# Kernel optimization log

Measured on AMD Instinct MI355X. Metric: run time of the kernel, lower is better.

The kernel has to match this reference:

```python
import jax, jax.numpy as jnp
import numpy as np

NEG_BIG = -9e15  # matches torch's -9000000000000000.0 mask value
LRELU_ALPHA = 0.2


def setup_inputs() -> dict:
    key = jax.random.key(0)
    ks = jax.random.split(key, 6)
    B, N, Fin, Fout = 2, 4096, 64, 64
    x = jax.random.normal(ks[0], (B, N, Fin), jnp.float32)
    pos = jax.random.normal(ks[1], (B, N, 3), jnp.float32)
    # xavier-ish scaled params
    W = jax.random.normal(ks[2], (Fin, Fout), jnp.float32) * (1.0 / np.sqrt(Fin))
    a = jax.random.normal(ks[3], (2 * Fout, 1), jnp.float32) * (1.0 / np.sqrt(2 * Fout))
    Wp = jax.random.normal(ks[4], (3, Fout), jnp.float32) * (1.0 / np.sqrt(3))
    bp = jnp.zeros((Fout,), jnp.float32)
    return {"x": x, "pos": pos, "W": W, "a": a, "Wp": Wp, "bp": bp, "k": 20}


def reference(x, pos, W, a, Wp, bp, k):
    B, N, _ = x.shape
    Fout = W.shape[1]
    Wh = x @ W  # [B,N,Fout]

    # Dynamic kNN graph (adj=None path): squared-distance ranking == cdist ranking
    sq = jnp.sum(pos * pos, axis=-1)  # [B,N]
    d2 = sq[:, :, None] + sq[:, None, :] - 2.0 * jnp.einsum('bnd,bmd->bnm', pos, pos)
    _, idx = jax.lax.top_k(-d2, k + 1)  # smallest k+1 distances
    idx = idx[:, :, 1:]  # drop self
    adj = jnp.zeros((B, N, N), x.dtype).at[
        jnp.arange(B)[:, None, None], jnp.arange(N)[None, :, None], idx
    ].set(1.0)

    # e[b,i,j] = leakyrelu(a1.Wh_i + a2.Wh_j); decompose instead of O(N^2*2F) concat
    f1 = Wh @ a[:Fout]  # [B,N,1]
    f2 = Wh @ a[Fout:]  # [B,N,1]
    e = f1 + jnp.swapaxes(f2, 1, 2)  # [B,N,N]
    e = jnp.where(e > 0, e, LRELU_ALPHA * e)

    e = jnp.where(adj > 0, e, NEG_BIG)
    attn = jax.nn.softmax(e, axis=2)  # dropout is identity in eval mode

    h = jnp.einsum('bnm,bmf->bnf', attn, Wh) + jax.nn.relu(pos @ Wp + bp)
    return jax.nn.elu(h)  # concat=True path
```

## Files before the change

kernel.cpp:

```cpp
#include <hip/hip_runtime.h>
#include <cfloat>

#define NB 4096
#define FD 64
#define EPT 16
#define LRELU_ALPHA 0.2f
#define CAND_CAP 512

__global__ __launch_bounds__(256) void prep_kernel(
    const float* __restrict__ x, const float* __restrict__ pos,
    const float* __restrict__ W, const float* __restrict__ a,
    const float* __restrict__ Wp, const float* __restrict__ bp,
    float* __restrict__ Wh, float* __restrict__ f1, float* __restrict__ f2,
    float* __restrict__ pp)
{
    __shared__ float sW[FD * FD];
    __shared__ float sa[2 * FD];
    const int tid = threadIdx.x;
    #pragma unroll
    for (int t = 0; t < 16; ++t) sW[tid + t * 256] = W[tid + t * 256];
    if (tid < 2 * FD) sa[tid] = a[tid];
    __syncthreads();

    const int wave = tid >> 6, lane = tid & 63;
    const int row = blockIdx.x * 4 + wave;

    const float xv = x[row * FD + lane];
    float acc = 0.f;
    #pragma unroll
    for (int i = 0; i < FD; ++i) {
        const float xi = __shfl(xv, i, 64);
        acc = fmaf(xi, sW[i * FD + lane], acc);
    }
    Wh[row * FD + lane] = acc;

    float r1 = acc * sa[lane];
    float r2 = acc * sa[FD + lane];
    #pragma unroll
    for (int off = 32; off > 0; off >>= 1) {
        r1 += __shfl_down(r1, off, 64);
        r2 += __shfl_down(r2, off, 64);
    }
    if (lane == 0) { f1[row] = r1; f2[row] = r2; }

    const float px = pos[row * 3 + 0];
    const float py = pos[row * 3 + 1];
    const float pz = pos[row * 3 + 2];
    float v = fmaf(px, Wp[0 * FD + lane],
             fmaf(py, Wp[1 * FD + lane],
             fmaf(pz, Wp[2 * FD + lane], bp[lane])));
    pp[row * FD + lane] = v > 0.f ? v : 0.f;
}

__device__ __forceinline__ unsigned long long shfl_xor_u64(unsigned long long v, int m) {
    int lo = __shfl_xor((int)(unsigned int)(v & 0xFFFFFFFFull), m, 64);
    int hi = __shfl_xor((int)(unsigned int)(v >> 32), m, 64);
    return ((unsigned long long)(unsigned int)hi << 32) | (unsigned int)lo;
}

__global__ __launch_bounds__(256) void gat_kernel(
    const float* __restrict__ pos, const float* __restrict__ Wh,
    const float* __restrict__ f1, const float* __restrict__ f2,
    const float* __restrict__ pp, const int* __restrict__ kptr,
    float* __restrict__ out)
{
    __shared__ unsigned long long wm[84];
    __shared__ unsigned long long cand[CAND_CAP];
    __shared__ unsigned long long sT;
    __shared__ unsigned int cnt;
    __shared__ int nidx[64];
    __shared__ float aw[64];
    __shared__ float part[4][FD];

    const int tid = threadIdx.x;
    const int lane = tid & 63, wave = tid >> 6;
    const int row = blockIdx.x;
    const int b = row >> 12, n = row & (NB - 1);
    const float* posb = pos + (size_t)b * NB * 3;

    if (tid == 0) cnt = 0;

    const float qx = posb[n * 3 + 0];
    const float qy = posb[n * 3 + 1];
    const float qz = posb[n * 3 + 2];
    const float sqn = __fadd_rn(__fadd_rn(__fmul_rn(qx, qx), __fmul_rn(qy, qy)),
                                __fmul_rn(qz, qz));

    unsigned int key[EPT];
    unsigned long long pmin = ~0ull;
    #pragma unroll
    for (int t = 0; t < EPT; ++t) {
        const int m = t * 256 + tid;
        const float px = posb[m * 3 + 0];
        const float py = posb[m * 3 + 1];
        const float pz = posb[m * 3 + 2];
        const float sqm = __fadd_rn(__fadd_rn(__fmul_rn(px, px), __fmul_rn(py, py)),
                                    __fmul_rn(pz, pz));
        const float dot = __fadd_rn(__fadd_rn(__fmul_rn(qx, px), __fmul_rn(qy, py)),
                                    __fmul_rn(qz, pz));
        const float d2 = __fsub_rn(__fadd_rn(sqn, sqm), __fmul_rn(2.0f, dot));
        const unsigned int u = __float_as_uint(d2);
        const unsigned int kk = u ^ ((unsigned int)((int)u >> 31) | 0x80000000u);
        key[t] = kk;
        const unsigned long long pk = ((unsigned long long)kk << 12) | (unsigned int)m;
        pmin = pk < pmin ? pk : pmin;
    }

    unsigned long long v = pmin;
    #pragma unroll
    for (int kk2 = 2; kk2 <= 64; kk2 <<= 1) {
        #pragma unroll
        for (int j = kk2 >> 1; j > 0; j >>= 1) {
            const unsigned long long o = shfl_xor_u64(v, j);
            const bool up = ((lane & kk2) == 0);
            const bool keepMin = (((lane & j) == 0) == up);
            const unsigned long long mn = v < o ? v : o;
            const unsigned long long mx = v < o ? o : v;
            v = keepMin ? mn : mx;
        }
    }
    if (lane < 21) wm[wave * 21 + lane] = v;
    __syncthreads();

    if (tid < 84) {
        const unsigned long long x = wm[tid];
        int r = 0;
        for (int j = 0; j < 84; ++j) r += (wm[j] < x);
        if (r == 20) sT = x;
    }
    __syncthreads();
    const unsigned long long T = sT;

    #pragma unroll
    for (int t = 0; t < EPT; ++t) {
        const int m = t * 256 + tid;
        const unsigned long long pk = ((unsigned long long)key[t] << 12) | (unsigned int)m;
        if (pk <= T) {
            const unsigned int p = atomicAdd(&cnt, 1u);
            if (p < CAND_CAP) cand[p] = pk;
        }
    }
    __syncthreads();

    const int k = *kptr;
    const int cn = cnt < (unsigned)CAND_CAP ? (int)cnt : CAND_CAP;
    const float f1n = f1[row];
    if (tid < cn) {
        const unsigned long long x = cand[tid];
        int r = 0;
        for (int j = 0; j < cn; ++j) r += (cand[j] < x);
        if (r >= 1 && r <= k) {
            const int m = (int)(x & 0xFFFu);
            nidx[r - 1] = m;
            float e = f1n + f2[(b << 12) + m];
            aw[r - 1] = e > 0.f ? e : LRELU_ALPHA * e;
        }
    }
    __syncthreads();

    if (tid == 0) {
        float mx = -FLT_MAX;
        for (int t = 0; t < k; ++t) mx = fmaxf(mx, aw[t]);
        float Z = 0.f;
        for (int t = 0; t < k; ++t) Z += __expf(aw[t] - mx);
        const float rz = 1.0f / Z;
        for (int t = 0; t < k; ++t) aw[t] = __expf(aw[t] - mx) * rz;
    }
    __syncthreads();

    const float* whb = Wh + ((size_t)(b << 12) << 6);
    float h = 0.f;
    for (int t = wave; t < k; t += 4)
        h = fmaf(aw[t], whb[((size_t)nidx[t] << 6) + lane], h);
    part[wave][lane] = h;
    __syncthreads();
    if (tid < FD) {
        float h2 = part[0][tid] + part[1][tid] + part[2][tid] + part[3][tid];
        h2 += pp[row * FD + tid];
        out[row * FD + tid] = h2 > 0.f ? h2 : expm1f(h2);
    }
}

extern "C" void kernel_launch(void* const* d_in, const int* in_sizes, int n_in,
                              void* d_out, int out_size, void* d_ws, size_t ws_size,
                              hipStream_t stream) {
    const float* x   = (const float*)d_in[0];
    const float* pos = (const float*)d_in[1];
    const float* W   = (const float*)d_in[2];
    const float* a   = (const float*)d_in[3];
    const float* Wp  = (const float*)d_in[4];
    const float* bp  = (const float*)d_in[5];
    const int*   kp  = (const int*)d_in[6];

    float* ws = (float*)d_ws;
    float* Wh = ws;
    float* f1 = Wh + 524288;
    float* f2 = f1 + 8192;
    float* pp = f2 + 8192;
    float* out = (float*)d_out;

    prep_kernel<<<2048, 256, 0, stream>>>(x, pos, W, a, Wp, bp, Wh, f1, f2, pp);
    gat_kernel<<<8192, 256, 0, stream>>>(pos, Wh, f1, f2, pp, kp, out);
}
```

Baseline: 126.8 us.

## Fuse projection into GAT kernel using linearity of attention aggregation

```diff
diff --git a/kernel.cpp b/kernel.cpp
--- a/kernel.cpp
+++ b/kernel.cpp
@@ -5,52 +5,7 @@
 #define FD 64
 #define EPT 16
 #define LRELU_ALPHA 0.2f
-#define CAND_CAP 512
-
-__global__ __launch_bounds__(256) void prep_kernel(
-    const float* __restrict__ x, const float* __restrict__ pos,
-    const float* __restrict__ W, const float* __restrict__ a,
-    const float* __restrict__ Wp, const float* __restrict__ bp,
-    float* __restrict__ Wh, float* __restrict__ f1, float* __restrict__ f2,
-    float* __restrict__ pp)
-{
-    __shared__ float sW[FD * FD];
-    __shared__ float sa[2 * FD];
-    const int tid = threadIdx.x;
-    #pragma unroll
-    for (int t = 0; t < 16; ++t) sW[tid + t * 256] = W[tid + t * 256];
-    if (tid < 2 * FD) sa[tid] = a[tid];
-    __syncthreads();
-
-    const int wave = tid >> 6, lane = tid & 63;
-    const int row = blockIdx.x * 4 + wave;
-
-    const float xv = x[row * FD + lane];
-    float acc = 0.f;
-    #pragma unroll
-    for (int i = 0; i < FD; ++i) {
-        const float xi = __shfl(xv, i, 64);
-        acc = fmaf(xi, sW[i * FD + lane], acc);
-    }
-    Wh[row * FD + lane] = acc;
-
-    float r1 = acc * sa[lane];
-    float r2 = acc * sa[FD + lane];
-    #pragma unroll
-    for (int off = 32; off > 0; off >>= 1) {
-        r1 += __shfl_down(r1, off, 64);
-        r2 += __shfl_down(r2, off, 64);
-    }
-    if (lane == 0) { f1[row] = r1; f2[row] = r2; }
-
-    const float px = pos[row * 3 + 0];
-    const float py = pos[row * 3 + 1];
-    const float pz = pos[row * 3 + 2];
-    float v = fmaf(px, Wp[0 * FD + lane],
-             fmaf(py, Wp[1 * FD + lane],
-             fmaf(pz, Wp[2 * FD + lane], bp[lane])));
-    pp[row * FD + lane] = v > 0.f ? v : 0.f;
-}
+#define CAND_CAP 256
 
 __device__ __forceinline__ unsigned long long shfl_xor_u64(unsigned long long v, int m) {
     int lo = __shfl_xor((int)(unsigned int)(v & 0xFFFFFFFFull), m, 64);
@@ -58,19 +13,26 @@
     return ((unsigned long long)(unsigned int)hi << 32) | (unsigned int)lo;
 }
 
-__global__ __launch_bounds__(256) void gat_kernel(
-    const float* __restrict__ pos, const float* __restrict__ Wh,
-    const float* __restrict__ f1, const float* __restrict__ f2,
-    const float* __restrict__ pp, const int* __restrict__ kptr,
-    float* __restrict__ out)
+__global__ __launch_bounds__(256) void gat_fused(
+    const float* __restrict__ x, const float* __restrict__ pos,
+    const float* __restrict__ W, const float* __restrict__ a,
+    const float* __restrict__ Wp, const float* __restrict__ bp,
+    const int* __restrict__ kptr, float* __restrict__ out)
 {
-    __shared__ unsigned long long wm[84];
-    __shared__ unsigned long long cand[CAND_CAP];
+    __shared__ float sW[FD * 65];
+    __shared__ unsigned long long upool[672];
+    __shared__ float sWa1[FD], sWa2[FD];
     __shared__ unsigned long long sT;
     __shared__ unsigned int cnt;
-    __shared__ int nidx[64];
-    __shared__ float aw[64];
+    __shared__ int idx21[32];
+    __shared__ float aw[32];
+    __shared__ float sf1;
+    __shared__ float gs[FD];
     __shared__ float part[4][FD];
+
+    unsigned long long* wm   = upool;
+    unsigned long long* cand = upool + 84;
+    float (*xs)[FD] = (float(*)[FD])upool;
 
     const int tid = threadIdx.x;
     const int lane = tid & 63, wave = tid >> 6;
@@ -78,6 +40,11 @@
     const int b = row >> 12, n = row & (NB - 1);
     const float* posb = pos + (size_t)b * NB * 3;
 
+    #pragma unroll
+    for (int t = 0; t < 16; ++t) {
+        const int e = t * 256 + tid;
+        sW[(e >> 6) * 65 + (e & 63)] = W[e];
+    }
     if (tid == 0) cnt = 0;
 
     const float qx = posb[n * 3 + 0];
@@ -123,10 +90,10 @@
     __syncthreads();
 
     if (tid < 84) {
-        const unsigned long long x = wm[tid];
+        const unsigned long long xv = wm[tid];
         int r = 0;
-        for (int j = 0; j < 84; ++j) r += (wm[j] < x);
-        if (r == 20) sT = x;
+        for (int j = 0; j < 84; ++j) r += (wm[j] < xv);
+        if (r == 20) sT = xv;
     }
     __syncthreads();
     const unsigned long long T = sT;
@@ -143,41 +110,81 @@
     __syncthreads();
 
     const int k = *kptr;
+    const int K1 = k + 1;
     const int cn = cnt < (unsigned)CAND_CAP ? (int)cnt : CAND_CAP;
-    const float f1n = f1[row];
     if (tid < cn) {
-        const unsigned long long x = cand[tid];
+        const unsigned long long xv = cand[tid];
         int r = 0;
-        for (int j = 0; j < cn; ++j) r += (cand[j] < x);
-        if (r >= 1 && r <= k) {
-            const int m = (int)(x & 0xFFFu);
-            nidx[r - 1] = m;
-            float e = f1n + f2[(b << 12) + m];
-            aw[r - 1] = e > 0.f ? e : LRELU_ALPHA * e;
+        for (int j = 0; j < cn; ++j) r += (cand[j] < xv);
+        if (r >= 1 && r <= k) idx21[r] = (int)(xv & 0xFFFu);
+    }
+    if (tid == 0) idx21[0] = n;
+    __syncthreads();
+
+    for (int t = wave; t < K1; t += 4)
+        xs[t][lane] = x[((size_t)((b << 12) + idx21[t]) << 6) + lane];
+    if (wave == 0) {
+        float s = 0.f;
+        #pragma unroll
+        for (int j = 0; j < FD; ++j) s = fmaf(sW[lane * 65 + j], a[j], s);
+        sWa1[lane] = s;
+    } else if (wave == 1) {
+        float s = 0.f;
+        #pragma unroll
+        for (int j = 0; j < FD; ++j) s = fmaf(sW[lane * 65 + j], a[FD + j], s);
+        sWa2[lane] = s;
+    }
+    __syncthreads();
+
+    for (int t = wave; t < K1; t += 4) {
+        const float* wa = (t == 0) ? sWa1 : sWa2;
+        float p = xs[t][lane] * wa[lane];
+        #pragma unroll
+        for (int off = 32; off > 0; off >>= 1) p += __shfl_down(p, off, 64);
+        if (lane == 0) { if (t == 0) sf1 = p; else aw[t] = p; }
+    }
+    __syncthreads();
+
+    if (tid == 0) {
+        const float f1v = sf1;
+        float mx = -FLT_MAX;
+        for (int t = 1; t <= k; ++t) {
+            float e = f1v + aw[t];
+            e = e > 0.f ? e : LRELU_ALPHA * e;
+            aw[t] = e;
+            mx = fmaxf(mx, e);
         }
-    }
-    __syncthreads();
-
-    if (tid == 0) {
-        float mx = -FLT_MAX;
-        for (int t = 0; t < k; ++t) mx = fmaxf(mx, aw[t]);
         float Z = 0.f;
-        for (int t = 0; t < k; ++t) Z += __expf(aw[t] - mx);
+        for (int t = 1; t <= k; ++t) Z += __expf(aw[t] - mx);
         const float rz = 1.0f / Z;
-        for (int t = 0; t < k; ++t) aw[t] = __expf(aw[t] - mx) * rz;
-    }
-    __syncthreads();
-
-    const float* whb = Wh + ((size_t)(b << 12) << 6);
-    float h = 0.f;
-    for (int t = wave; t < k; t += 4)
-        h = fmaf(aw[t], whb[((size_t)nidx[t] << 6) + lane], h);
-    part[wave][lane] = h;
-    __syncthreads();
+        for (int t = 1; t <= k; ++t) aw[t] = __expf(aw[t] - mx) * rz;
+    }
+    __syncthreads();
+
+    float gp = 0.f;
+    for (int t = 1 + wave; t <= k; t += 4)
+        gp = fmaf(aw[t], xs[t][lane], gp);
+    part[wave][lane] = gp;
+    __syncthreads();
+    if (tid < FD) gs[tid] = part[0][tid] + part[1][tid] + part[2][tid] + part[3][tid];
+    __syncthreads();
+
+    float hp = 0.f;
+    #pragma unroll
+    for (int i = 0; i < 16; ++i) {
+        const int kk = wave * 16 + i;
+        hp = fmaf(gs[kk], sW[kk * 65 + lane], hp);
+    }
+    part[wave][lane] = hp;
+    __syncthreads();
+
     if (tid < FD) {
-        float h2 = part[0][tid] + part[1][tid] + part[2][tid] + part[3][tid];
-        h2 += pp[row * FD + tid];
-        out[row * FD + tid] = h2 > 0.f ? h2 : expm1f(h2);
+        float h = part[0][tid] + part[1][tid] + part[2][tid] + part[3][tid];
+        float pv = fmaf(qx, Wp[0 * FD + tid],
+                   fmaf(qy, Wp[1 * FD + tid],
+                   fmaf(qz, Wp[2 * FD + tid], bp[tid])));
+        h += pv > 0.f ? pv : 0.f;
+        out[((size_t)row << 6) + tid] = h > 0.f ? h : expm1f(h);
     }
 }
 
@@ -191,14 +198,7 @@
     const float* Wp  = (const float*)d_in[4];
     const float* bp  = (const float*)d_in[5];
     const int*   kp  = (const int*)d_in[6];
-
-    float* ws = (float*)d_ws;
-    float* Wh = ws;
-    float* f1 = Wh + 524288;
-    float* f2 = f1 + 8192;
-    float* pp = f2 + 8192;
     float* out = (float*)d_out;
 
-    prep_kernel<<<2048, 256, 0, stream>>>(x, pos, W, a, Wp, bp, Wh, f1, f2, pp);
-    gat_kernel<<<8192, 256, 0, stream>>>(pos, Wh, f1, f2, pp, kp, out);
+    gat_fused<<<8192, 256, 0, stream>>>(x, pos, W, a, Wp, bp, kp, out);
 }
```

New measurement: 194.8 us. +53.6%, slower.
